# Kernel tuning notes

Measured on AMD Instinct MI355X. Metric: run time of the kernel, lower is better.

The kernel has to match this reference:

```python
import jax, jax.numpy as jnp
import numpy as np

B, W, D = 8, 1024, 1024
HEADS, KDIM, VDIM = 16, 64, 64


def setup_inputs() -> dict:
    key = jax.random.key(0)
    k1, k2, k3, k4 = jax.random.split(key, 4)
    # he_normal-ish scaling for weights
    s = (2.0 / D) ** 0.5
    return {
        "inputs": jax.random.normal(k1, (B, W, D), dtype=jnp.float32),
        "Wq": jax.random.normal(k2, (D, HEADS * KDIM), dtype=jnp.float32) * s,
        "Wk": jax.random.normal(k3, (D, HEADS * KDIM), dtype=jnp.float32) * s,
        "Wv": jax.random.normal(k4, (D, HEADS * VDIM), dtype=jnp.float32) * s,
    }


def reference(inputs, Wq, Wk, Wv):
    # Self-attention: memory = inputs
    bsz, win, _ = inputs.shape
    # DenseHeads: linear projection, reshaped to (B, W, heads, head_units)
    q = (inputs @ Wq).reshape(bsz, win, HEADS, KDIM)
    k = (inputs @ Wk).reshape(bsz, win, HEADS, KDIM)
    v = (inputs @ Wv).reshape(bsz, win, HEADS, VDIM)
    scale = KDIM ** (-0.5)
    # scores[b,q,h,m] = sum_k Q[b,q,h,k] * K[b,m,h,k]
    scores = jnp.einsum("bqhk,bmhk->bqhm", q, k) * scale
    attn = jax.nn.softmax(scores, axis=-1)
    # out[b,q,h,v] = sum_m attn[b,q,h,m] * V[b,m,h,v]
    out = jnp.einsum("bqhm,bmhv->bqhv", attn, v)
    return out
```

## Files before the change

kernel.cpp:

```cpp
#include <hip/hip_runtime.h>
#include <stdint.h>


using bf16x8 = __attribute__((ext_vector_type(8))) __bf16;
using f32x4  = __attribute__((ext_vector_type(4))) float;
using f16x4  = __attribute__((ext_vector_type(4))) _Float16;

union frag_u  { uint4 u4; bf16x8 f; };
union vfrag_u { uint2 u2; f16x4 f; };
union pfrag_u { unsigned int u[2]; f16x4 f; };

__device__ inline unsigned short f2bf(float x){
  unsigned int u = __float_as_uint(x);
  u += 0x7fffu + ((u >> 16) & 1u);
  return (unsigned short)(u >> 16);
}

__device__ inline unsigned int pkrtz_u32(float a, float b){
  auto r = __builtin_amdgcn_cvt_pkrtz(a, b);
  unsigned int u; __builtin_memcpy(&u, &r, 4); return u;
}

__device__ inline void gl_lds16(const void* g, void* l){
  __builtin_amdgcn_global_load_lds(
      (const __attribute__((address_space(1))) void*)g,
      (__attribute__((address_space(3))) void*)l, 16, 0, 0);
}

#define SBAR() do{ asm volatile("" ::: "memory"); __builtin_amdgcn_s_barrier(); asm volatile("" ::: "memory"); }while(0)
#define VMC(n)  asm volatile("s_waitcnt vmcnt(" #n ")" ::: "memory")

__global__ void cast_all(const float* __restrict__ X,
                         const float* __restrict__ Wq, const float* __restrict__ Wk,
                         const float* __restrict__ Wv,
                         unsigned short* __restrict__ Xb,
                         unsigned short* __restrict__ Wt){
  __shared__ float tile[64][65];
  int bid = blockIdx.x;
  if (bid < 8192){
    int i = (bid * 256 + threadIdx.x) * 4;
    float4 v = *(const float4*)(X + i);
    ushort4 o;
    o.x = f2bf(v.x); o.y = f2bf(v.y); o.z = f2bf(v.z); o.w = f2bf(v.w);
    *(ushort4*)(Xb + i) = o;
    return;
  }
  int id = bid - 8192;
  int proj = id >> 8;
  int rem  = id & 255;
  int kt = rem & 15, nt = rem >> 4;
  const float* Wsrc = (proj == 0) ? Wq : ((proj == 1) ? Wk : Wv);
  int k0 = kt * 64, n0 = nt * 64;
  int tx = threadIdx.x & 63, ty = threadIdx.x >> 6;
  for (int i = 0; i < 16; i++){
    int k = i * 4 + ty;
    tile[k][tx] = Wsrc[(k0 + k) * 1024 + n0 + tx];
  }
  __syncthreads();
  for (int i = 0; i < 16; i++){
    int n = i * 4 + ty;
    Wt[(proj * 1024 + n0 + n) * 1024 + k0 + tx] = f2bf(tile[tx][n]);
  }
}

__global__ __launch_bounds__(1024, 4) void gemm_qkv(
    const unsigned short* __restrict__ Xb,
    const unsigned short* __restrict__ Wt,
    unsigned short* __restrict__ QK,
    unsigned short* __restrict__ Vt){
  __shared__ __align__(16) char Abuf[2][32768];
  __shared__ __align__(16) char Bbuf[2][24576];

  int bid = blockIdx.x;
  int tau = (bid & 7) * 64 + (bid >> 3);
  int by = tau >> 4, bx = tau & 15;
  int tid = threadIdx.x;
  int w = tid >> 6, lane = tid & 63;
  int li = lane & 15, g = lane >> 4;
  int lrow = lane >> 3;
  int wr = w >> 2, wc = w & 3;
  int wu = __builtin_amdgcn_readfirstlane(w);

  int xcol = ((lane & 7) ^ lrow) << 3;
  int aoff0 = (by * 256 + w * 8 + lrow) * 1024 + xcol;
  int aoff1 = (by * 256 + (16 + w) * 8 + lrow) * 1024 + xcol;
  int bseg0 = (w < 8) ? w : (w + 8);
  int bseg1 = w + 8;
  int boff0 = (bx * 192 + bseg0 * 8 + lrow) * 1024 + xcol;
  int boff1 = (bx * 192 + bseg1 * 8 + lrow) * 1024 + xcol;

  int swz  = (li & 7) << 4;
  int colA0 = (g * 16) ^ swz;
  int colA1 = (64 + g * 16) ^ swz;
  int aBase = (wr * 64 + li) * 128;
  int bBase = (wc * 48 + li) * 128;

  f32x4 acc[4][3] = {};
  frag_u bfr[3][2], af[2][2];

#define LDB(buf) do{ \
  _Pragma("unroll") for (int n = 0; n < 3; n++){ \
    bfr[n][0].u4 = *(const uint4*)&Bbuf[buf][bBase + n * 2048 + colA0]; \
    bfr[n][1].u4 = *(const uint4*)&Bbuf[buf][bBase + n * 2048 + colA1]; } }while(0)
#define LDA2(buf, m0) do{ \
  af[0][0].u4 = *(const uint4*)&Abuf[buf][aBase + (m0)     * 2048 + colA0]; \
  af[0][1].u4 = *(const uint4*)&Abuf[buf][aBase + (m0)     * 2048 + colA1]; \
  af[1][0].u4 = *(const uint4*)&Abuf[buf][aBase + (m0 + 1) * 2048 + colA0]; \
  af[1][1].u4 = *(const uint4*)&Abuf[buf][aBase + (m0 + 1) * 2048 + colA1]; }while(0)
#define MFMA6(P) do{ __builtin_amdgcn_s_setprio(1); \
  _Pragma("unroll") for (int kk = 0; kk < 2; kk++) \
  _Pragma("unroll") for (int i = 0; i < 2; i++) \
  _Pragma("unroll") for (int n = 0; n < 3; n++) \
    acc[(P) + i][n] = __builtin_amdgcn_mfma_f32_16x16x32_bf16( \
        af[i][kk].f, bfr[n][kk].f, acc[(P) + i][n], 0, 0, 0); \
  __builtin_amdgcn_s_setprio(0); }while(0)

  gl_lds16(Wt + boff0, &Bbuf[0][bseg0 * 1024]);
  if (wu < 8) gl_lds16(Wt + boff1, &Bbuf[0][bseg1 * 1024]);
  gl_lds16(Xb + aoff0, &Abuf[0][w * 1024]);
  gl_lds16(Xb + aoff1, &Abuf[0][(16 + w) * 1024]);
  gl_lds16(Wt + boff0 + 64, &Bbuf[1][bseg0 * 1024]);
  if (wu < 8){
    gl_lds16(Wt + boff1 + 64, &Bbuf[1][bseg1 * 1024]);
    VMC(2);
  } else {
    VMC(1);
  }
  SBAR();

  for (int t = 0; t < 16; ++t){
    int cur = t & 1, nxt = cur ^ 1;
    LDB(cur);
    LDA2(cur, 0);
    if (t < 15){
      gl_lds16(Xb + aoff0 + (t + 1) * 64, &Abuf[nxt][w * 1024]);
      gl_lds16(Xb + aoff1 + (t + 1) * 64, &Abuf[nxt][(16 + w) * 1024]);
    }
    MFMA6(0);
    SBAR();
    LDA2(cur, 2);
    if (t < 14){
      gl_lds16(Wt + boff0 + (t + 2) * 64, &Bbuf[cur][bseg0 * 1024]);
      if (wu < 8) gl_lds16(Wt + boff1 + (t + 2) * 64, &Bbuf[cur][bseg1 * 1024]);
    }
    MFMA6(2);
    if (t < 14){
      if (wu < 8) { VMC(2); } else { VMC(1); }
    } else if (t == 14) {
      VMC(0);
    }
    SBAR();
  }
#undef LDB
#undef LDA2
#undef MFMA6

  int row0 = by * 256 + wr * 64 + g * 4;
  int bb16 = (by >> 2) * 16;
#pragma unroll
  for (int n = 0; n < 3; n++){
    int cb = bx * 192 + wc * 48 + n * 16;
    if (cb < 2048){
      float sc = (cb < 1024) ? 0.1803368801111f : 1.0f;
#pragma unroll
      for (int m = 0; m < 4; m++){
        int row = row0 + m * 16;
#pragma unroll
        for (int r = 0; r < 4; r++)
          QK[(size_t)(row + r) * 2048 + cb + li] = f2bf(acc[m][n][r] * sc);
      }
    } else {
      int vc = cb + li - 2048;
      int hh = vc >> 6, dd = vc & 63;
#pragma unroll
      for (int m = 0; m < 4; m++){
        int mtok = (row0 + m * 16) & 1023;
        uint2 cv;
        cv.x = pkrtz_u32(acc[m][n][0], acc[m][n][1]);
        cv.y = pkrtz_u32(acc[m][n][2], acc[m][n][3]);
        *(uint2*)(Vt + ((size_t)(bb16 + hh) * 64 + dd) * 1024 + mtok) = cv;
      }
    }
  }
}

__global__ __launch_bounds__(256, 4) void attn(const unsigned short* __restrict__ QK,
                                               const unsigned short* __restrict__ Vt,
                                               float* __restrict__ Out){
  __shared__ __align__(16) unsigned short Kbuf[64 * 64];
  __shared__ __align__(16) unsigned short Vbuf[64 * 64];
  int id = blockIdx.x;
  int bh = id & 127, qb = id >> 7;
  int b = bh >> 4, h = bh & 15;
  int w = threadIdx.x >> 6, lane = threadIdx.x & 63;
  int g = lane >> 4, li = lane & 15;
  int lrow = lane >> 3, lcol = lane & 7;
  int scol = ((lcol ^ lrow) & 7) * 8;

  frag_u qf[2];
  {
    int tok = b * 1024 + qb * 64 + w * 16 + li;
    const unsigned short* qp = QK + (size_t)tok * 2048 + h * 64 + g * 8;
    qf[0].u4 = *(const uint4*)(qp);
    qf[1].u4 = *(const uint4*)(qp + 32);
  }

  f32x4 o[4] = {};
  f32x4 osum = {};
  const f32x4 bias = {-10.f, -10.f, -10.f, -10.f};
  pfrag_u ones;
  ones.u[0] = 0x3c003c00u; ones.u[1] = 0x3c003c00u;

  const unsigned short* Kg = QK + (size_t)b * 1024 * 2048 + 1024 + h * 64;
  const unsigned short* Vg = Vt + (size_t)bh * 65536;

  for (int mt = 0; mt < 16; mt++){
    int m0 = mt * 64;
    __syncthreads();
    for (int i = 0; i < 2; i++){
      int idx = w * 2 + i;
      int row = idx * 8 + lrow;
      gl_lds16(Kg + (size_t)(m0 + row) * 2048 + scol, Kbuf + idx * 512);
      gl_lds16(Vg + row * 1024 + m0 + scol,           Vbuf + idx * 512);
    }
    __syncthreads();

    f32x4 s[4];
    for (int t = 0; t < 4; t++) s[t] = bias;
    for (int t = 0; t < 4; t++){
      for (int c = 0; c < 2; c++){
        frag_u kf;
        kf.u4 = *(const uint4*)(Kbuf + (t * 16 + li) * 64 + ((((c << 2) + g) ^ (li & 7)) << 3));
        s[t] = __builtin_amdgcn_mfma_f32_16x16x32_bf16(kf.f, qf[c].f, s[t], 0, 0, 0);
      }
    }

    pfrag_u pf[4];
    for (int t = 0; t < 4; t++){
      float p0 = __builtin_exp2f(s[t][0]);
      float p1 = __builtin_exp2f(s[t][1]);
      float p2 = __builtin_exp2f(s[t][2]);
      float p3 = __builtin_exp2f(s[t][3]);
      pf[t].u[0] = pkrtz_u32(p0, p1);
      pf[t].u[1] = pkrtz_u32(p2, p3);
    }

    for (int t = 0; t < 4; t++)
      osum = __builtin_amdgcn_mfma_f32_16x16x16f16(ones.f, pf[t].f, osum, 0, 0, 0);
    for (int tv = 0; tv < 4; tv++){
      for (int t = 0; t < 4; t++){
        int gg = ((t * 2 + (g >> 1)) ^ (li & 7));
        vfrag_u vf;
        vf.u2 = *(const uint2*)(Vbuf + (tv * 16 + li) * 64 + gg * 8 + (g & 1) * 4);
        o[tv] = __builtin_amdgcn_mfma_f32_16x16x16f16(vf.f, pf[t].f, o[tv], 0, 0, 0);
      }
    }
  }

  float inv = 1.f / osum[0];

  int tok = b * 1024 + qb * 64 + w * 16 + li;
  float* op = Out + (size_t)tok * 1024 + h * 64 + g * 4;
  for (int tv = 0; tv < 4; tv++){
    float4 v4;
    v4.x = o[tv][0] * inv; v4.y = o[tv][1] * inv;
    v4.z = o[tv][2] * inv; v4.w = o[tv][3] * inv;
    *(float4*)(op + tv * 16) = v4;
  }
}

extern "C" void kernel_launch(void* const* d_in, const int* in_sizes, int n_in,
                              void* d_out, int out_size, void* d_ws, size_t ws_size,
                              hipStream_t stream) {
  const float* X  = (const float*)d_in[0];
  const float* Wq = (const float*)d_in[1];
  const float* Wk = (const float*)d_in[2];
  const float* Wv = (const float*)d_in[3];
  float* Out = (float*)d_out;
  char* ws = (char*)d_ws;
  unsigned short* Xb = (unsigned short*)(ws);
  unsigned short* Wt = (unsigned short*)(ws + (size_t)16 * 1024 * 1024);
  unsigned short* QK = (unsigned short*)(ws + (size_t)22 * 1024 * 1024);
  unsigned short* Vt = (unsigned short*)(ws + (size_t)54 * 1024 * 1024);

  cast_all<<<8960, 256, 0, stream>>>(X, Wq, Wk, Wv, Xb, Wt);
  gemm_qkv<<<512, 1024, 0, stream>>>(Xb, Wt, QK, Vt);
  attn    <<<2048, 256, 0, stream>>>(QK, Vt, Out);
}
```

Measured before the change: 208.1 us.

## Process two query sub-tiles per wave to reuse K/V tiles

Each wave now computes 32 query rows instead of 16, sharing every K and V fragment loaded from LDS across two query sub-tiles. The grid is halved, so each K/V tile is fetched from global memory into LDS half as often per query. This cuts global traffic and LDS reads per MFMA, at the cost of doubled accumulator and score registers, which may pressure occupancy under the launch bounds.

```diff
diff --git a/kernel.cpp b/kernel.cpp
--- a/kernel.cpp
+++ b/kernel.cpp
@@ -197,16 +197,17 @@
   int lrow = lane >> 3, lcol = lane & 7;
   int scol = ((lcol ^ lrow) & 7) * 8;
 
-  frag_u qf[2];
-  {
-    int tok = b * 1024 + qb * 64 + w * 16 + li;
+  frag_u qf[2][2];
+#pragma unroll
+  for (int u = 0; u < 2; u++){
+    int tok = b * 1024 + qb * 128 + w * 32 + u * 16 + li;
     const unsigned short* qp = QK + (size_t)tok * 2048 + h * 64 + g * 8;
-    qf[0].u4 = *(const uint4*)(qp);
-    qf[1].u4 = *(const uint4*)(qp + 32);
-  }
-
-  f32x4 o[4] = {};
-  f32x4 osum = {};
+    qf[u][0].u4 = *(const uint4*)(qp);
+    qf[u][1].u4 = *(const uint4*)(qp + 32);
+  }
+
+  f32x4 o[2][4] = {};
+  f32x4 osum[2] = {};
   const f32x4 bias = {-10.f, -10.f, -10.f, -10.f};
   pfrag_u ones;
   ones.u[0] = 0x3c003c00u; ones.u[1] = 0x3c003c00u;
@@ -225,47 +226,66 @@
     }
     __syncthreads();
 
-    f32x4 s[4];
-    for (int t = 0; t < 4; t++) s[t] = bias;
+    f32x4 s[2][4];
+#pragma unroll
+    for (int u = 0; u < 2; u++)
+#pragma unroll
+      for (int t = 0; t < 4; t++) s[u][t] = bias;
+#pragma unroll
     for (int t = 0; t < 4; t++){
+#pragma unroll
       for (int c = 0; c < 2; c++){
         frag_u kf;
         kf.u4 = *(const uint4*)(Kbuf + (t * 16 + li) * 64 + ((((c << 2) + g) ^ (li & 7)) << 3));
-        s[t] = __builtin_amdgcn_mfma_f32_16x16x32_bf16(kf.f, qf[c].f, s[t], 0, 0, 0);
-      }
-    }
-
-    pfrag_u pf[4];
+        s[0][t] = __builtin_amdgcn_mfma_f32_16x16x32_bf16(kf.f, qf[0][c].f, s[0][t], 0, 0, 0);
+        s[1][t] = __builtin_amdgcn_mfma_f32_16x16x32_bf16(kf.f, qf[1][c].f, s[1][t], 0, 0, 0);
+      }
+    }
+
+    pfrag_u pf[2][4];
+#pragma unroll
+    for (int u = 0; u < 2; u++){
+#pragma unroll
+      for (int t = 0; t < 4; t++){
+        float p0 = __builtin_exp2f(s[u][t][0]);
+        float p1 = __builtin_exp2f(s[u][t][1]);
+        float p2 = __builtin_exp2f(s[u][t][2]);
+        float p3 = __builtin_exp2f(s[u][t][3]);
+        pf[u][t].u[0] = pkrtz_u32(p0, p1);
+        pf[u][t].u[1] = pkrtz_u32(p2, p3);
+      }
+    }
+
+#pragma unroll
     for (int t = 0; t < 4; t++){
-      float p0 = __builtin_exp2f(s[t][0]);
-      float p1 = __builtin_exp2f(s[t][1]);
-      float p2 = __builtin_exp2f(s[t][2]);
-      float p3 = __builtin_exp2f(s[t][3]);
-      pf[t].u[0] = pkrtz_u32(p0, p1);
-      pf[t].u[1] = pkrtz_u32(p2, p3);
-    }
-
-    for (int t = 0; t < 4; t++)
-      osum = __builtin_amdgcn_mfma_f32_16x16x16f16(ones.f, pf[t].f, osum, 0, 0, 0);
+      osum[0] = __builtin_amdgcn_mfma_f32_16x16x16f16(ones.f, pf[0][t].f, osum[0], 0, 0, 0);
+      osum[1] = __builtin_amdgcn_mfma_f32_16x16x16f16(ones.f, pf[1][t].f, osum[1], 0, 0, 0);
+    }
+#pragma unroll
     for (int tv = 0; tv < 4; tv++){
+#pragma unroll
       for (int t = 0; t < 4; t++){
         int gg = ((t * 2 + (g >> 1)) ^ (li & 7));
         vfrag_u vf;
         vf.u2 = *(const uint2*)(Vbuf + (tv * 16 + li) * 64 + gg * 8 + (g & 1) * 4);
-        o[tv] = __builtin_amdgcn_mfma_f32_16x16x16f16(vf.f, pf[t].f, o[tv], 0, 0, 0);
-      }
-    }
-  }
-
-  float inv = 1.f / osum[0];
-
-  int tok = b * 1024 + qb * 64 + w * 16 + li;
-  float* op = Out + (size_t)tok * 1024 + h * 64 + g * 4;
-  for (int tv = 0; tv < 4; tv++){
-    float4 v4;
-    v4.x = o[tv][0] * inv; v4.y = o[tv][1] * inv;
-    v4.z = o[tv][2] * inv; v4.w = o[tv][3] * inv;
-    *(float4*)(op + tv * 16) = v4;
+        o[0][tv] = __builtin_amdgcn_mfma_f32_16x16x16f16(vf.f, pf[0][t].f, o[0][tv], 0, 0, 0);
+        o[1][tv] = __builtin_amdgcn_mfma_f32_16x16x16f16(vf.f, pf[1][t].f, o[1][tv], 0, 0, 0);
+      }
+    }
+  }
+
+#pragma unroll
+  for (int u = 0; u < 2; u++){
+    float inv = 1.f / osum[u][0];
+    int tok = b * 1024 + qb * 128 + w * 32 + u * 16 + li;
+    float* op = Out + (size_t)tok * 1024 + h * 64 + g * 4;
+#pragma unroll
+    for (int tv = 0; tv < 4; tv++){
+      float4 v4;
+      v4.x = o[u][tv][0] * inv; v4.y = o[u][tv][1] * inv;
+      v4.z = o[u][tv][2] * inv; v4.w = o[u][tv][3] * inv;
+      *(float4*)(op + tv * 16) = v4;
+    }
   }
 }
 
@@ -285,5 +305,5 @@
 
   cast_all<<<8960, 256, 0, stream>>>(X, Wq, Wk, Wv, Xb, Wt);
   gemm_qkv<<<512, 1024, 0, stream>>>(Xb, Wt, QK, Vt);
-  attn    <<<2048, 256, 0, stream>>>(QK, Vt, Out);
-}
+  attn    <<<1024, 256, 0, stream>>>(QK, Vt, Out);
+}
```

After: 208.3 us. Within noise of the previous version (+0.1%).
